# Kernel optimization log

Measured on AMD Instinct MI355X. Metric: run time of the kernel, lower is better.

The kernel has to match this reference:

```python
import jax, jax.numpy as jnp
import numpy as np

# ---- static configuration (mirrors TimeFold init + deterministic prepare()) ----
B = 256
F = 512            # fft_length//2 + 1
T = 81             # input STFT frames
WIN = 1022         # window_length == frame_length == fft_length
HOP = 400          # hop_length
SEG = 1000         # segment_length
OVL = 50           # overlap_length
TO_HOP = 100       # deterministic choice of randint(1, hop_size=100)
SIG_LEN = (T - 1) * HOP + WIN            # 33022, inverse_stft output length

# prepare(): t segments kept, gaps of TO_HOP deleted
_t = SIG_LEN // (SEG + TO_HOP)
if SIG_LEN % (SEG + TO_HOP) >= SEG:
    _t += 1                               # _t = 30
KEPT_LEN = _t * SEG                       # 30000
OUT_LEN = SEG + (_t - 1) * (SEG - OVL)    # 28550
NF = 1 + (OUT_LEN - WIN) // HOP           # 69 output STFT frames

# indices kept after deleting the to_hop gaps (complement of delete_indices)
KEEP_IDX = np.concatenate([k * (SEG + TO_HOP) + np.arange(SEG) for k in range(_t)])

# overlap-add blending coefficients (length KEPT_LEN), built exactly as in prepare()
_ramp_up = np.arange(1, OVL + 1, dtype=np.float32) / OVL
_ramp_dn = np.arange(OVL, 0, -1, dtype=np.float32) / OVL
COEFF_INC = np.pad(np.tile(np.pad(_ramp_up, (0, SEG - OVL)), _t - 1), (SEG - OVL, OVL))
COEFF_DEC = np.pad(np.tile(np.pad(_ramp_dn, (SEG - OVL, 0)), _t - 1), (0, SEG))
_c = np.tile(np.pad(np.ones(SEG - 2 * OVL, np.float32), (OVL, OVL)), _t - 2)
_c = np.pad(np.pad(_c, (OVL, 0)), (SEG - OVL, 0), constant_values=1.0)
_c = np.pad(np.pad(_c, (0, OVL)), (0, SEG - OVL), constant_values=1.0)
COEFF_CONST = _c.astype(np.float32)

# final_delete_indices: drop [k*SEG, k*SEG+OVL) for k = 1.._t-1
_mask = np.ones(KEPT_LEN, bool)
for k in range(1, _t):
    _mask[k * SEG:k * SEG + OVL] = False
FINAL_KEEP = np.nonzero(_mask)[0]         # length OUT_LEN

# gather index grids for framing (static)
ISTFT_IDX = np.arange(T)[:, None] * HOP + np.arange(WIN)[None, :]
STFT_IDX = np.arange(NF)[:, None] * HOP + np.arange(WIN)[None, :]


def _hann(n):
    # periodic Hann, matches tf.signal.hann_window(periodic=True)
    return (0.5 - 0.5 * jnp.cos(2.0 * jnp.pi * jnp.arange(n, dtype=jnp.float32) / n)).astype(jnp.float32)


def _synthesis_window():
    w = _hann(WIN)
    denom = w * w
    overlaps = -(-WIN // HOP)
    denom = jnp.pad(denom, (0, overlaps * HOP - WIN))
    denom = denom.reshape(overlaps, HOP).sum(axis=0)
    denom = jnp.tile(denom, overlaps)[:WIN]
    return w / denom


def setup_inputs() -> dict:
    key = jax.random.key(0)
    x = jax.random.normal(key, (B, F, T, 2), dtype=jnp.float32)
    return {"x": x}


def reference(x) -> jnp.ndarray:
    # x: [B, 512, T, 2] real/imag STFT
    stfts = jax.lax.complex(x[..., 0], x[..., 1])          # [B, F, T]
    frames = jnp.transpose(stfts, (0, 2, 1))               # [B, T, F]
    # inverse_stft: irfft each frame, apply synthesis window, overlap-add
    tf_frames = jnp.fft.irfft(frames, n=WIN, axis=-1)
    tf_frames = tf_frames * _synthesis_window()
    sig = jnp.zeros((x.shape[0], SIG_LEN), jnp.float32).at[:, ISTFT_IDX].add(tf_frames)
    # dynamic segment delete (gather of kept indices)
    kept = sig[:, KEEP_IDX]                                # [B, KEPT_LEN]
    # shifted copy: drop first OVL samples, zero-pad at end
    shifted = jnp.concatenate(
        [kept[:, OVL:], jnp.zeros((x.shape[0], OVL), jnp.float32)], axis=1)
    # weighted overlap-add blend
    out = (jnp.asarray(COEFF_CONST) + jnp.asarray(COEFF_DEC)) * kept \
        + jnp.asarray(COEFF_INC) * shifted
    out = out[:, FINAL_KEEP]                               # [B, OUT_LEN]
    # forward STFT (periodic Hann, no padding)
    fr = out[:, STFT_IDX] * _hann(WIN)
    S = jnp.fft.rfft(fr, n=WIN, axis=-1)                   # [B, NF, 512]
    S = jnp.transpose(S, (0, 2, 1))                        # [B, 512, NF]
    return jnp.stack([S.real, S.imag], axis=-1)            # [B, 512, NF, 2]
```

## Files before the change

### kernel.cpp

```cpp
#include <hip/hip_runtime.h>
#include <math.h>

typedef unsigned short u16;
typedef unsigned int u32;

#define B_   256
#define F_   512
#define T_   81
#define WIN_ 1022
#define HOP_ 400
#define NF_  69
#define OUT_LEN_ 28550
#define SEG_ 1000
#define OVL_ 50

#define MA_  20736
#define MB_  17664
#define K_   1024
#define NMT_A 81
#define NMT_B 69

#define BASA_B     0u
#define BASB_B     (BASA_B + 2097152u)
#define ABUF_B     (BASB_B + 2097152u)
#define TF_B       (ABUF_B + 42467328u)
#define OUTF_B     (TF_B + 42467328u)
#define OUTF_STRIDE_ 28672

typedef __attribute__((ext_vector_type(8))) short bf8_t;
typedef __attribute__((ext_vector_type(4))) float f4_t;
typedef const __attribute__((address_space(1))) void* as1cv;
typedef __attribute__((address_space(3))) void* as3v;

__device__ __forceinline__ float b2f(u16 v) {
  u32 u = ((u32)v) << 16; float f; __builtin_memcpy(&f, &u, 4); return f;
}
__device__ __forceinline__ u16 f2b(float f) {
  u32 u; __builtin_memcpy(&u, &f, 4);
  return (u16)((u + 0x7fffu + ((u >> 16) & 1u)) >> 16);
}

__global__ __launch_bounds__(256) void gen_basisA(u16* __restrict__ BA) {
  int n = blockIdx.x;
  const float twopi_N = 6.283185307179586f / (float)WIN_;
  float scale = 0.f;
  if (n < WIN_) {
    float w = 0.5f - 0.5f * cosf(twopi_N * (float)n);
    int j = n % HOP_;
    float a = 0.5f - 0.5f * cosf(twopi_N * (float)j);
    float b = 0.5f - 0.5f * cosf(twopi_N * (float)(j + 400));
    float d = a * a + b * b;
    if (j + 800 < WIN_) {
      float c2 = 0.5f - 0.5f * cosf(twopi_N * (float)(j + 800));
      d += c2 * c2;
    }
    scale = (w / d) * (1.0f / (float)WIN_);
  }
  for (int k = threadIdx.x; k < 512; k += 256) {
    int m = (k * n) % WIN_;
    float ang = twopi_N * (float)m;
    float s, c; __sincosf(ang, &s, &c);
    bool edge = (k == 0) || (k == 511);
    float ck = edge ? 1.f : 2.f;
    float re = scale * ck * c;
    float im = edge ? 0.f : -scale * ck * s;
    BA[(size_t)n * K_ + 2 * k]     = f2b(re);
    BA[(size_t)n * K_ + 2 * k + 1] = f2b(im);
  }
}

__global__ __launch_bounds__(256) void gen_basisB(u16* __restrict__ BB) {
  int k = blockIdx.x;
  const float twopi_N = 6.283185307179586f / (float)WIN_;
  for (int w = threadIdx.x; w < K_; w += 256) {
    float re = 0.f, im = 0.f;
    if (w < WIN_) {
      int m = (k * w) % WIN_;
      float ang = twopi_N * (float)m;
      float s, c; __sincosf(ang, &s, &c);
      float h = 0.5f - 0.5f * cosf(twopi_N * (float)w);
      re = h * c; im = -h * s;
    }
    BB[(size_t)(2 * k)     * K_ + w] = f2b(re);
    BB[(size_t)(2 * k + 1) * K_ + w] = f2b(im);
  }
}

__global__ __launch_bounds__(256) void prep1(const float* __restrict__ x,
                                             u16* __restrict__ Abuf) {
  __shared__ float2 tile[32][33];
  int k0 = blockIdx.x * 32, t0 = blockIdx.y * 32, b = blockIdx.z;
  int c = threadIdx.x & 31, rr = threadIdx.x >> 5;
  const float2* xp = (const float2*)x;
#pragma unroll
  for (int i = 0; i < 4; ++i) {
    int k = k0 + rr + 8 * i, t = t0 + c;
    float2 v = make_float2(0.f, 0.f);
    if (t < T_) v = xp[(size_t)(b * F_ + k) * T_ + t];
    tile[rr + 8 * i][c] = v;
  }
  __syncthreads();
#pragma unroll
  for (int i = 0; i < 4; ++i) {
    int t = t0 + rr + 8 * i, kc = c;
    if (t < T_) {
      float2 v = tile[kc][rr + 8 * i];
      u32 packed = (u32)f2b(v.x) | ((u32)f2b(v.y) << 16);
      *(u32*)&Abuf[(size_t)(b * T_ + t) * K_ + 2 * (k0 + kc)] = packed;
    }
  }
}

template <int EPI>
__global__ __launch_bounds__(512, 4) void gemm_bf16(const u16* __restrict__ A,
                                                    const u16* __restrict__ Bt,
                                                    void* __restrict__ Cout) {
  __shared__ u16 sA[3][8192];
  __shared__ u16 sB[3][4096];
  const int tid = threadIdx.x;
  const int lane = tid & 63, wv = tid >> 6;
  const int wm = wv >> 1, wn = wv & 1;
  const int fr = lane & 15, fq = lane >> 4;

  const int chunk = (EPI == 0) ? NMT_A : NMT_B;
  int id = blockIdx.x;
  int wgid = (id & 7) * chunk + (id >> 3);
  const int mt = wgid >> 3, nt = wgid & 7;
  const int bm = mt * 256, bn = nt * 128;

  const u16 *pA0, *pA1;
  if (EPI == 0) {
    pA0 = A + (size_t)(bm + 16 * wv + fr) * K_ + fq * 8;
    pA1 = A + (size_t)(bm + 16 * (wv + 8) + fr) * K_ + fq * 8;
  } else {
    int m0 = bm + 16 * wv + fr;
    int b0 = m0 / NF_, f0 = m0 - b0 * NF_;
    pA0 = A + (size_t)b0 * OUTF_STRIDE_ + f0 * HOP_ + fq * 8;
    int m1 = m0 + 128;
    int b1 = m1 / NF_, f1 = m1 - b1 * NF_;
    pA1 = A + (size_t)b1 * OUTF_STRIDE_ + f1 * HOP_ + fq * 8;
  }
  const u16* pB0 = Bt + (size_t)(bn + 16 * wv + fr) * K_ + fq * 8;

  f4_t acc[4][4];
#pragma unroll
  for (int i = 0; i < 4; ++i)
#pragma unroll
    for (int j = 0; j < 4; ++j) acc[i][j] = (f4_t){0.f, 0.f, 0.f, 0.f};

  auto STAGE = [&](int t) {
    const int buf = t % 3;
    const int ko = t * 32;
    __builtin_amdgcn_global_load_lds((as1cv)(const void*)(pA0 + ko),
                                     (as3v)(&sA[buf][(wv)     * 512]), 16, 0, 0);
    __builtin_amdgcn_global_load_lds((as1cv)(const void*)(pA1 + ko),
                                     (as3v)(&sA[buf][(wv + 8) * 512]), 16, 0, 0);
    __builtin_amdgcn_global_load_lds((as1cv)(const void*)(pB0 + ko),
                                     (as3v)(&sB[buf][(wv)     * 512]), 16, 0, 0);
  };

  STAGE(0);
  STAGE(1);
  asm volatile("s_waitcnt vmcnt(3)" ::: "memory");
  __builtin_amdgcn_s_barrier();

#pragma unroll
  for (int t = 0; t < 32; ++t) {
    const int buf = t % 3;
    bf8_t a[4], b[4];
#pragma unroll
    for (int i = 0; i < 4; ++i)
      a[i] = *(const bf8_t*)&sA[buf][(wm * 4 + i) * 512 + lane * 8];
#pragma unroll
    for (int j = 0; j < 4; ++j)
      b[j] = *(const bf8_t*)&sB[buf][(wn * 4 + j) * 512 + lane * 8];

    if (t + 2 < 32) STAGE(t + 2);

    __builtin_amdgcn_s_setprio(1);
#pragma unroll
    for (int i = 0; i < 4; ++i)
#pragma unroll
      for (int j = 0; j < 4; ++j)
        acc[i][j] = __builtin_amdgcn_mfma_f32_16x16x32_bf16(a[i], b[j], acc[i][j], 0, 0, 0);
    __builtin_amdgcn_s_setprio(0);

    if (t + 1 < 32) {
      if (t + 2 < 32) asm volatile("s_waitcnt vmcnt(3) lgkmcnt(0)" ::: "memory");
      else            asm volatile("s_waitcnt vmcnt(0) lgkmcnt(0)" ::: "memory");
      __builtin_amdgcn_s_barrier();
    }
  }

  const int wmr = wm * 64, wnc = wn * 64;
  if (EPI == 0) {
    u16* C = (u16*)Cout;
#pragma unroll
    for (int i = 0; i < 4; ++i)
#pragma unroll
      for (int j = 0; j < 4; ++j) {
        int colg = bn + wnc + 16 * j + fr;
#pragma unroll
        for (int r = 0; r < 4; ++r) {
          int rowg = bm + wmr + 16 * i + fq * 4 + r;
          C[(size_t)rowg * K_ + colg] = f2b(acc[i][j][r]);
        }
      }
  } else {
    float* out = (float*)Cout;
    __syncthreads();
    float* ep = (float*)((char*)&sA[0][0] + wv * 4096);
    int m = bm + wmr + lane;
    int b = m / NF_;
    int f = m - b * NF_;
    for (int j = 0; j < 4; ++j) {
#pragma unroll
      for (int i = 0; i < 4; ++i)
#pragma unroll
        for (int r = 0; r < 4; ++r) {
          int row64 = 16 * i + fq * 4 + r;
          ep[row64 * 16 + fr] = acc[i][j][r];
        }
      int colbase = bn + wnc + 16 * j;
#pragma unroll
      for (int a2 = 0; a2 < 8; ++a2) {
        int k = (colbase >> 1) + a2;
        float2 v = make_float2(ep[lane * 16 + 2 * a2], ep[lane * 16 + 2 * a2 + 1]);
        ((float2*)out)[((size_t)b * F_ + k) * NF_ + f] = v;
      }
    }
  }
}

__device__ __forceinline__ float sigval(const u16* __restrict__ tfb, int i) {
  int t1 = i / HOP_; if (t1 > T_ - 1) t1 = T_ - 1;
  int t0 = (i >= WIN_) ? (i - (WIN_ - 1) + HOP_ - 1) / HOP_ : 0;
  float acc = 0.f;
  for (int t = t0; t <= t1; ++t)
    acc += b2f(tfb[(size_t)t * K_ + (i - t * HOP_)]);
  return acc;
}

__global__ __launch_bounds__(256) void k3_fold(const u16* __restrict__ tf,
                                               u16* __restrict__ outf) {
  int id = blockIdx.x * 256 + threadIdx.x;
  if (id >= B_ * OUT_LEN_) return;
  int b = id / OUT_LEN_;
  int p = id - b * OUT_LEN_;
  int s, r;
  if (p < SEG_) { s = 0; r = p; }
  else {
    int q = p - SEG_;
    s = q / (SEG_ - OVL_) + 1;
    r = OVL_ + (q - (s - 1) * (SEG_ - OVL_));
  }
  const u16* tfb = tf + (size_t)b * T_ * K_;
  float val;
  if (r >= SEG_ - OVL_ && s <= 28) {
    float dec = (float)(SEG_ - r) * (1.f / (float)OVL_);
    float inc = (float)(r - (SEG_ - OVL_ - 1)) * (1.f / (float)OVL_);
    float v1 = sigval(tfb, s * 1100 + r);
    float v2 = sigval(tfb, (s + 1) * 1100 + (r - (SEG_ - OVL_)));
    val = dec * v1 + inc * v2;
  } else {
    val = sigval(tfb, s * 1100 + r);
  }
  outf[(size_t)b * OUTF_STRIDE_ + p] = f2b(val);
}

extern "C" void kernel_launch(void* const* d_in, const int* in_sizes, int n_in,
                              void* d_out, int out_size, void* d_ws, size_t ws_size,
                              hipStream_t stream) {
  const float* x = (const float*)d_in[0];
  char* ws = (char*)d_ws;
  u16* BA   = (u16*)(ws + BASA_B);
  u16* BB   = (u16*)(ws + BASB_B);
  u16* Abuf = (u16*)(ws + ABUF_B);
  u16* TF   = (u16*)(ws + TF_B);
  u16* outf = (u16*)(ws + OUTF_B);

  hipLaunchKernelGGL(gen_basisA, dim3(1024), dim3(256), 0, stream, BA);
  hipLaunchKernelGGL(gen_basisB, dim3(512), dim3(256), 0, stream, BB);
  hipLaunchKernelGGL(prep1, dim3(16, 3, 256), dim3(256), 0, stream, x, Abuf);
  hipLaunchKernelGGL((gemm_bf16<0>), dim3(NMT_A * 8), dim3(512), 0, stream,
                     Abuf, BA, (void*)TF);
  int n3 = B_ * OUT_LEN_;
  hipLaunchKernelGGL(k3_fold, dim3((n3 + 255) / 256), dim3(256), 0, stream, TF, outf);
  hipLaunchKernelGGL((gemm_bf16<1>), dim3(NMT_B * 8), dim3(512), 0, stream,
                     outf, BB, (void*)d_out);
}
```

Before: 313.2 us.

## Enlarge GEMM tiles to 256x256 with 4-stage split A/B pipeline

The bf16 GEMM tile grows from 256x128 to 256x256, so each wave now holds an 8x4 accumulator array. The LDS ring buffer goes from 3 to 4 stages, and A and B loads are issued in separate halves interleaved with two MFMA phases per k-step. Block-to-XCD remapping now handles uneven block counts. The aim is more data reuse per loaded byte and better overlap of loads with compute. The cost is higher register and LDS use, which lowers occupancy to 2 blocks per CU, plus more barriers per iteration.

```diff
diff --git a/kernel.cpp b/kernel.cpp
--- a/kernel.cpp
+++ b/kernel.cpp
@@ -17,8 +17,8 @@
 #define MA_  20736
 #define MB_  17664
 #define K_   1024
-#define NMT_A 81
-#define NMT_B 69
+#define NBLK0 324
+#define NBLK1 276
 
 #define BASA_B     0u
 #define BASB_B     (BASA_B + 2097152u)
@@ -112,21 +112,22 @@
 }
 
 template <int EPI>
-__global__ __launch_bounds__(512, 4) void gemm_bf16(const u16* __restrict__ A,
+__global__ __launch_bounds__(512, 2) void gemm_bf16(const u16* __restrict__ A,
                                                     const u16* __restrict__ Bt,
                                                     void* __restrict__ Cout) {
-  __shared__ u16 sA[3][8192];
-  __shared__ u16 sB[3][4096];
+  __shared__ u16 sAB[4][16384];
   const int tid = threadIdx.x;
   const int lane = tid & 63, wv = tid >> 6;
-  const int wm = wv >> 1, wn = wv & 1;
+  const int wm = wv >> 2, wn = wv & 3;
   const int fr = lane & 15, fq = lane >> 4;
 
-  const int chunk = (EPI == 0) ? NMT_A : NMT_B;
-  int id = blockIdx.x;
-  int wgid = (id & 7) * chunk + (id >> 3);
-  const int mt = wgid >> 3, nt = wgid & 7;
-  const int bm = mt * 256, bn = nt * 128;
+  const int nwg = (EPI == 0) ? NBLK0 : NBLK1;
+  const int q = nwg >> 3, r = nwg & 7;
+  int orig = blockIdx.x;
+  int xcd = orig & 7, pos = orig >> 3;
+  int wgid = (xcd < r ? xcd * (q + 1) : r * (q + 1) + (xcd - r) * q) + pos;
+  const int mt = wgid >> 2, nt = wgid & 3;
+  const int bm = mt * 256, bn = nt * 256;
 
   const u16 *pA0, *pA1;
   if (EPI == 0) {
@@ -141,92 +142,117 @@
     pA1 = A + (size_t)b1 * OUTF_STRIDE_ + f1 * HOP_ + fq * 8;
   }
   const u16* pB0 = Bt + (size_t)(bn + 16 * wv + fr) * K_ + fq * 8;
-
-  f4_t acc[4][4];
-#pragma unroll
-  for (int i = 0; i < 4; ++i)
+  const u16* pB1 = Bt + (size_t)(bn + 16 * (wv + 8) + fr) * K_ + fq * 8;
+
+  f4_t acc[8][4];
+#pragma unroll
+  for (int i = 0; i < 8; ++i)
 #pragma unroll
     for (int j = 0; j < 4; ++j) acc[i][j] = (f4_t){0.f, 0.f, 0.f, 0.f};
 
-  auto STAGE = [&](int t) {
-    const int buf = t % 3;
+  auto STAGE_A = [&](int t) {
+    const int buf = t & 3;
     const int ko = t * 32;
     __builtin_amdgcn_global_load_lds((as1cv)(const void*)(pA0 + ko),
-                                     (as3v)(&sA[buf][(wv)     * 512]), 16, 0, 0);
+                                     (as3v)(&sAB[buf][(wv)     * 512]), 16, 0, 0);
     __builtin_amdgcn_global_load_lds((as1cv)(const void*)(pA1 + ko),
-                                     (as3v)(&sA[buf][(wv + 8) * 512]), 16, 0, 0);
+                                     (as3v)(&sAB[buf][(wv + 8) * 512]), 16, 0, 0);
+  };
+  auto STAGE_B = [&](int t) {
+    const int buf = t & 3;
+    const int ko = t * 32;
     __builtin_amdgcn_global_load_lds((as1cv)(const void*)(pB0 + ko),
-                                     (as3v)(&sB[buf][(wv)     * 512]), 16, 0, 0);
+                                     (as3v)(&sAB[buf][8192 + (wv)     * 512]), 16, 0, 0);
+    __builtin_amdgcn_global_load_lds((as1cv)(const void*)(pB1 + ko),
+                                     (as3v)(&sAB[buf][8192 + (wv + 8) * 512]), 16, 0, 0);
   };
 
-  STAGE(0);
-  STAGE(1);
-  asm volatile("s_waitcnt vmcnt(3)" ::: "memory");
+  STAGE_A(0); STAGE_B(0);
+  STAGE_A(1); STAGE_B(1);
+  STAGE_A(2); STAGE_B(2);
+  asm volatile("s_waitcnt vmcnt(8)" ::: "memory");
   __builtin_amdgcn_s_barrier();
 
 #pragma unroll
   for (int t = 0; t < 32; ++t) {
-    const int buf = t % 3;
-    bf8_t a[4], b[4];
-#pragma unroll
-    for (int i = 0; i < 4; ++i)
-      a[i] = *(const bf8_t*)&sA[buf][(wm * 4 + i) * 512 + lane * 8];
-#pragma unroll
-    for (int j = 0; j < 4; ++j)
-      b[j] = *(const bf8_t*)&sB[buf][(wn * 4 + j) * 512 + lane * 8];
-
-    if (t + 2 < 32) STAGE(t + 2);
-
+    const int buf = t & 3;
+    const u16* sA = &sAB[buf][0];
+    const u16* sB = &sAB[buf][8192];
+    bf8_t a[8], b[4];
+
+#pragma unroll
+    for (int i = 0; i < 8; ++i)
+      a[i] = *(const bf8_t*)&sA[(wm * 8 + i) * 512 + lane * 8];
+#pragma unroll
+    for (int j = 0; j < 2; ++j)
+      b[j] = *(const bf8_t*)&sB[(wn * 4 + j) * 512 + lane * 8];
+    if (t + 3 < 32) STAGE_A(t + 3);
+    __builtin_amdgcn_s_barrier();
+    asm volatile("s_waitcnt lgkmcnt(0)" ::: "memory");
     __builtin_amdgcn_s_setprio(1);
 #pragma unroll
-    for (int i = 0; i < 4; ++i)
-#pragma unroll
-      for (int j = 0; j < 4; ++j)
+    for (int i = 0; i < 8; ++i)
+#pragma unroll
+      for (int j = 0; j < 2; ++j)
         acc[i][j] = __builtin_amdgcn_mfma_f32_16x16x32_bf16(a[i], b[j], acc[i][j], 0, 0, 0);
     __builtin_amdgcn_s_setprio(0);
-
-    if (t + 1 < 32) {
-      if (t + 2 < 32) asm volatile("s_waitcnt vmcnt(3) lgkmcnt(0)" ::: "memory");
-      else            asm volatile("s_waitcnt vmcnt(0) lgkmcnt(0)" ::: "memory");
-      __builtin_amdgcn_s_barrier();
-    }
-  }
-
-  const int wmr = wm * 64, wnc = wn * 64;
+    __builtin_amdgcn_s_barrier();
+
+#pragma unroll
+    for (int j = 2; j < 4; ++j)
+      b[j] = *(const bf8_t*)&sB[(wn * 4 + j) * 512 + lane * 8];
+    if (t + 3 < 32) STAGE_B(t + 3);
+    __builtin_amdgcn_s_barrier();
+    asm volatile("s_waitcnt lgkmcnt(0)" ::: "memory");
+    __builtin_amdgcn_s_setprio(1);
+#pragma unroll
+    for (int i = 0; i < 8; ++i)
+#pragma unroll
+      for (int j = 2; j < 4; ++j)
+        acc[i][j] = __builtin_amdgcn_mfma_f32_16x16x32_bf16(a[i], b[j], acc[i][j], 0, 0, 0);
+    __builtin_amdgcn_s_setprio(0);
+
+    if (t < 29)       asm volatile("s_waitcnt vmcnt(8)" ::: "memory");
+    else if (t == 29) asm volatile("s_waitcnt vmcnt(4)" ::: "memory");
+    else if (t == 30) asm volatile("s_waitcnt vmcnt(0)" ::: "memory");
+    if (t < 31) __builtin_amdgcn_s_barrier();
+  }
+
   if (EPI == 0) {
     u16* C = (u16*)Cout;
 #pragma unroll
-    for (int i = 0; i < 4; ++i)
+    for (int i = 0; i < 8; ++i)
 #pragma unroll
       for (int j = 0; j < 4; ++j) {
-        int colg = bn + wnc + 16 * j + fr;
-#pragma unroll
-        for (int r = 0; r < 4; ++r) {
-          int rowg = bm + wmr + 16 * i + fq * 4 + r;
-          C[(size_t)rowg * K_ + colg] = f2b(acc[i][j][r]);
+        int colg = bn + wn * 64 + 16 * j + fr;
+#pragma unroll
+        for (int rr = 0; rr < 4; ++rr) {
+          int rowg = bm + wm * 128 + 16 * i + fq * 4 + rr;
+          C[(size_t)rowg * K_ + colg] = f2b(acc[i][j][rr]);
         }
       }
   } else {
     float* out = (float*)Cout;
-    __syncthreads();
-    float* ep = (float*)((char*)&sA[0][0] + wv * 4096);
-    int m = bm + wmr + lane;
-    int b = m / NF_;
-    int f = m - b * NF_;
+    float* ep = (float*)((char*)&sAB[0][0] + wv * 8192);
     for (int j = 0; j < 4; ++j) {
 #pragma unroll
-      for (int i = 0; i < 4; ++i)
-#pragma unroll
-        for (int r = 0; r < 4; ++r) {
-          int row64 = 16 * i + fq * 4 + r;
-          ep[row64 * 16 + fr] = acc[i][j][r];
+      for (int i = 0; i < 8; ++i)
+#pragma unroll
+        for (int rr = 0; rr < 4; ++rr)
+          ep[(16 * i + fq * 4 + rr) * 16 + fr] = acc[i][j][rr];
+      asm volatile("s_waitcnt lgkmcnt(0)" ::: "memory");
+      int colbase = bn + wn * 64 + 16 * j;
+#pragma unroll
+      for (int rr = 0; rr < 2; ++rr) {
+        int row = lane + rr * 64;
+        int m = bm + wm * 128 + row;
+        int bb = m / NF_, ff = m - bb * NF_;
+#pragma unroll
+        for (int a2 = 0; a2 < 8; ++a2) {
+          int k = (colbase >> 1) + a2;
+          float2 v = make_float2(ep[row * 16 + 2 * a2], ep[row * 16 + 2 * a2 + 1]);
+          ((float2*)out)[((size_t)bb * F_ + k) * NF_ + ff] = v;
         }
-      int colbase = bn + wnc + 16 * j;
-#pragma unroll
-      for (int a2 = 0; a2 < 8; ++a2) {
-        int k = (colbase >> 1) + a2;
-        float2 v = make_float2(ep[lane * 16 + 2 * a2], ep[lane * 16 + 2 * a2 + 1]);
-        ((float2*)out)[((size_t)b * F_ + k) * NF_ + f] = v;
       }
     }
   }
@@ -282,10 +308,10 @@
   hipLaunchKernelGGL(gen_basisA, dim3(1024), dim3(256), 0, stream, BA);
   hipLaunchKernelGGL(gen_basisB, dim3(512), dim3(256), 0, stream, BB);
   hipLaunchKernelGGL(prep1, dim3(16, 3, 256), dim3(256), 0, stream, x, Abuf);
-  hipLaunchKernelGGL((gemm_bf16<0>), dim3(NMT_A * 8), dim3(512), 0, stream,
+  hipLaunchKernelGGL((gemm_bf16<0>), dim3(NBLK0), dim3(512), 0, stream,
                      Abuf, BA, (void*)TF);
   int n3 = B_ * OUT_LEN_;
   hipLaunchKernelGGL(k3_fold, dim3((n3 + 255) / 256), dim3(256), 0, stream, TF, outf);
-  hipLaunchKernelGGL((gemm_bf16<1>), dim3(NMT_B * 8), dim3(512), 0, stream,
+  hipLaunchKernelGGL((gemm_bf16<1>), dim3(NBLK1), dim3(512), 0, stream,
                      outf, BB, (void*)d_out);
 }
```

New measurement: 315.5 us. About the same (+0.7%).
